# Performance work log

Hardware: AMD Instinct MI355X
Metric: run time of the kernel (lower is better)

The kernel has to match this reference:

```python
import jax, jax.numpy as jnp
import numpy as np
from math import sqrt

B, H, S, D = 4, 16, 2048, 64
NEG = -1000000000.0

def setup_inputs() -> dict:
    key = jax.random.key(0)
    kq, kk, kv, km = jax.random.split(key, 4)
    Q = jax.random.normal(kq, (B, H, S, D), dtype=jnp.float32)
    K = jax.random.normal(kk, (B, H, S, D), dtype=jnp.float32)
    V = jax.random.normal(kv, (B, H, S, D), dtype=jnp.float32)
    mask = jax.random.uniform(km, (B, 1, S, S)) < 0.1
    return {"Q": Q, "K": K, "V": V, "mask": mask}

def reference(Q, K, V, mask) -> jnp.ndarray:
    # scores: [B,H,S,S]
    scores = jnp.einsum('bhqd,bhkd->bhqk', Q, K)
    scores = jnp.where(mask, NEG, scores)
    attn = jax.nn.softmax(scores / sqrt(Q.shape[-1]), axis=-1)
    return jnp.einsum('bhqk,bhkd->bhqd', attn, V)
```

## Files before the change

kernel.cpp:

```cpp
#include <hip/hip_runtime.h>


#define SEQ 2048
#define DIM 64
#define NBH 64
#define LOG2E 1.44269504088896340736f
#define SCL (0.125f * LOG2E)
#define NEG_SCALED -1.25e8f

typedef short bf16x8 __attribute__((ext_vector_type(8)));
typedef float f32x4 __attribute__((ext_vector_type(4)));
typedef float f32x16 __attribute__((ext_vector_type(16)));

static __device__ __forceinline__ unsigned short f2bf(float f) {
    unsigned int u = __float_as_uint(f);
    u += 0x7fffu + ((u >> 16) & 1u);
    return (unsigned short)(u >> 16);
}

#define GLD16(gp, lp) __builtin_amdgcn_global_load_lds( \
    (const __attribute__((address_space(1))) unsigned int*)(gp), \
    (__attribute__((address_space(3))) unsigned int*)(lp), 16, 0, 0)

__global__ __launch_bounds__(256)
void prep_all_kernel(const float* __restrict__ K, const float* __restrict__ V,
                     const int* __restrict__ M,
                     unsigned short* __restrict__ Kb, unsigned short* __restrict__ Vt,
                     unsigned int* __restrict__ Mpt) {
    const int x = blockIdx.x;
    const int t = threadIdx.x;
    if (x < 4096) {
        size_t i0 = ((size_t)x * 256 + t) * 8;
        float4 a = *(const float4*)(K + i0);
        float4 b = *(const float4*)(K + i0 + 4);
        union { uint4 u; unsigned short s[8]; } w;
        w.s[0] = f2bf(a.x); w.s[1] = f2bf(a.y); w.s[2] = f2bf(a.z); w.s[3] = f2bf(a.w);
        w.s[4] = f2bf(b.x); w.s[5] = f2bf(b.y); w.s[6] = f2bf(b.z); w.s[7] = f2bf(b.w);
        *(uint4*)(Kb + i0) = w.u;
    } else if (x < 6144) {
        __shared__ __align__(16) unsigned short T[64 * 64];
        const int vb = x - 4096;
        const int bh = vb >> 5;
        const int k0 = (vb & 31) * 64;
        {
            const int kk = t >> 2;
            const int c  = t & 3;
            const int u  = (kk & ~12) | ((kk & 4) << 1) | ((kk & 8) >> 1);
            const int cs = c ^ ((u >> 3) & 3);
            const float* vp = V + ((size_t)bh * SEQ + k0 + kk) * DIM + c * 16;
            union { uint4 q[2]; unsigned short s[16]; } w;
            #pragma unroll
            for (int j = 0; j < 16; ++j) w.s[j] = f2bf(vp[j]);
            *(uint4*)&T[u * 64 + cs * 16]     = w.q[0];
            *(uint4*)&T[u * 64 + cs * 16 + 8] = w.q[1];
        }
        __syncthreads();
        {
            const int kc = t & 7;
            const int dp = t >> 3;
            const int ch = (dp >> 3) ^ (kc & 3);
            const unsigned int* T32 = (const unsigned int*)T;
            union { uint4 u; unsigned short s[8]; } o0, o1;
            #pragma unroll
            for (int i = 0; i < 8; ++i) {
                unsigned int v = T32[(8 * kc + i) * 32 + ch * 8 + (dp & 7)];
                o0.s[i] = (unsigned short)v;
                o1.s[i] = (unsigned short)(v >> 16);
            }
            unsigned short* op = Vt + ((size_t)bh * DIM + 2 * dp) * SEQ + k0 + 8 * kc;
            *(uint4*)op         = o0.u;
            *(uint4*)(op + SEQ) = o1.u;
        }
    } else {
        __shared__ unsigned int Wt[64][8];
        const int m  = x - 6144;
        const int b  = m >> 8;
        const int q0 = ((m >> 3) & 31) * 64;
        const int k0 = (m & 7) * 256;
        const int w  = t >> 6, l = t & 63;
        #pragma unroll 4
        for (int row = 0; row < 16; ++row) {
            const int q = q0 + w * 16 + row;
            int4 v4 = *(const int4*)(M + ((size_t)b * SEQ + q) * SEQ + k0 + l * 4);
            unsigned int nib = (unsigned int)(v4.x != 0) | ((unsigned int)(v4.y != 0) << 1)
                             | ((unsigned int)(v4.z != 0) << 2) | ((unsigned int)(v4.w != 0) << 3);
            unsigned int v = nib << (4 * (l & 7));
            v |= __shfl_xor(v, 1);
            v |= __shfl_xor(v, 2);
            v |= __shfl_xor(v, 4);
            if ((l & 7) == 0) Wt[w * 16 + row][l >> 3] = v;
        }
        __syncthreads();
        {
            const int q = t & 63, g0 = t >> 6;
            #pragma unroll
            for (int gg = 0; gg < 2; ++gg) {
                const int g = g0 + gg * 4;
                Mpt[((size_t)b * 64 + (k0 >> 5) + g) * SEQ + q0 + q] = Wt[q][g];
            }
        }
    }
}

__global__ __launch_bounds__(256, 4)
void attn_main_kernel(const float* __restrict__ Q,
                      const unsigned short* __restrict__ Kb,
                      const unsigned short* __restrict__ Vt,
                      const unsigned int* __restrict__ Mpt,
                      float* __restrict__ O)
{
    const int bh   = blockIdx.y;
    const int b    = bh >> 4;
    const int q0   = blockIdx.x * 128;
    const int tid  = threadIdx.x;
    const int wave = tid >> 6;
    const int lane = tid & 63;
    const int h    = lane >> 5;
    const int q32  = lane & 31;

    __shared__ __align__(16) unsigned short Kt[2][32 * 64];
    __shared__ __align__(16) unsigned short Vs[2][64 * 32];

    const unsigned short* Kbh = Kb + (size_t)bh * SEQ * DIM;
    const unsigned short* Vbh = Vt + (size_t)bh * SEQ * DIM;

    bf16x8 qf[4];
    {
        const float* qp = Q + ((size_t)bh * SEQ + q0 + wave * 32 + q32) * DIM + h * 8;
        #pragma unroll
        for (int dc = 0; dc < 4; ++dc) {
            float4 xx = *(const float4*)(qp + dc * 16);
            float4 yy = *(const float4*)(qp + dc * 16 + 4);
            qf[dc][0] = (short)f2bf(xx.x * SCL); qf[dc][1] = (short)f2bf(xx.y * SCL);
            qf[dc][2] = (short)f2bf(xx.z * SCL); qf[dc][3] = (short)f2bf(xx.w * SCL);
            qf[dc][4] = (short)f2bf(yy.x * SCL); qf[dc][5] = (short)f2bf(yy.y * SCL);
            qf[dc][6] = (short)f2bf(yy.z * SCL); qf[dc][7] = (short)f2bf(yy.w * SCL);
        }
    }

    const int kkey  = wave * 8 + (lane >> 3);
    const int kclog = (lane & 7) ^ (lane >> 3);
    const unsigned short* kg = Kbh + (size_t)kkey * DIM + kclog * 8;
    const int vd    = wave * 16 + (lane >> 2);
    const int vclog = (lane & 3) ^ ((lane >> 3) & 3);
    const unsigned short* vg = Vbh + (size_t)vd * SEQ + vclog * 8;
    unsigned short* kl[2] = { &Kt[0][wave * 512], &Kt[1][wave * 512] };
    unsigned short* vl[2] = { &Vs[0][wave * 512], &Vs[1][wave * 512] };

    const unsigned int* mp = Mpt + (size_t)b * 64 * SEQ + (q0 + wave * 32 + q32);

    f32x16 acc[2];
    #pragma unroll
    for (int i = 0; i < 16; ++i) { acc[0][i] = 0.f; acc[1][i] = 0.f; }
    float lsum = 0.f;

    GLD16(kg, kl[0]);
    GLD16(vg, vl[0]);

    #pragma unroll 2
    for (int it = 0; it < SEQ / 32; ++it) {
        __syncthreads();

        unsigned int mw = mp[it * SEQ];

        if (it + 1 < SEQ / 32) {
            const unsigned short* kgn = kg + (size_t)(it + 1) * 32 * DIM;
            const unsigned short* vgn = vg + (size_t)(it + 1) * 32;
            int nb = (it + 1) & 1;
            GLD16(kgn, kl[nb]);
            GLD16(vgn, vl[nb]);
        }

        const unsigned short* Ktb = Kt[it & 1];
        const unsigned short* Vsb = Vs[it & 1];

        f32x16 sc;
        #pragma unroll
        for (int i = 0; i < 16; ++i) sc[i] = 0.f;
        #pragma unroll
        for (int dc = 0; dc < 4; ++dc) {
            const int pos = (dc * 2 + h) ^ (q32 & 7);
            bf16x8 kf = *(const bf16x8*)(Ktb + q32 * 64 + pos * 8);
            sc = __builtin_amdgcn_mfma_f32_32x32x16_bf16(kf, qf[dc], sc, 0, 0, 0);
        }

        const unsigned int mq = mw >> (4 * h);
        float pv[16];
        #pragma unroll
        for (int r = 0; r < 16; ++r) {
            const int s = (r & 3) + 8 * (r >> 2);
            float e = __builtin_amdgcn_exp2f(sc[r]);
            pv[r] = ((mq >> s) & 1u) ? 0.f : e;
            lsum += pv[r];
        }
        unsigned int pk[8];
        #pragma unroll
        for (int m = 0; m < 8; ++m) {
            unsigned int u0 = __float_as_uint(pv[2 * m])     + 0x8000u;
            unsigned int u1 = __float_as_uint(pv[2 * m + 1]) + 0x8000u;
            pk[m] = __builtin_amdgcn_perm(u1, u0, 0x07060302u);
        }

        #pragma unroll
        for (int kk = 0; kk < 2; ++kk) {
            union { unsigned int u[4]; bf16x8 v; } fr;
            fr.u[0] = pk[4 * kk + 0];
            fr.u[1] = pk[4 * kk + 1];
            fr.u[2] = pk[4 * kk + 2];
            fr.u[3] = pk[4 * kk + 3];
            #pragma unroll
            for (int dh = 0; dh < 2; ++dh) {
                const int d   = dh * 32 + q32;
                const int pos = (kk * 2 + h) ^ ((q32 >> 1) & 3);
                bf16x8 vf = *(const bf16x8*)(Vsb + d * 32 + pos * 8);
                acc[dh] = __builtin_amdgcn_mfma_f32_32x32x16_bf16(vf, fr.v, acc[dh], 0, 0, 0);
            }
        }
    }

    lsum += __shfl_xor(lsum, 32);
    const float inv = 1.f / lsum;
    float* orow = O + ((size_t)bh * SEQ + q0 + wave * 32 + q32) * DIM;
    #pragma unroll
    for (int dh = 0; dh < 2; ++dh) {
        #pragma unroll
        for (int r23 = 0; r23 < 4; ++r23) {
            float4 w;
            w.x = acc[dh][4 * r23 + 0] * inv;
            w.y = acc[dh][4 * r23 + 1] * inv;
            w.z = acc[dh][4 * r23 + 2] * inv;
            w.w = acc[dh][4 * r23 + 3] * inv;
            *(float4*)(orow + dh * 32 + r23 * 8 + h * 4) = w;
        }
    }
}

__global__ __launch_bounds__(256)
void attn_fallback_kernel(const float* __restrict__ Q,
                          const float* __restrict__ K,
                          const float* __restrict__ V,
                          const int* __restrict__ mask,
                          float* __restrict__ O)
{
    const int bh   = blockIdx.y;
    const int b    = bh >> 4;
    const int q0   = blockIdx.x * 64;
    const int tid  = threadIdx.x;
    const int wave = tid >> 6;
    const int lane = tid & 63;
    const int quad = lane >> 4;
    const int l16  = lane & 15;

    __shared__ __align__(16) unsigned short Klds[32][72];
    __shared__ __align__(16) unsigned short VT[64][40];
    __shared__ __align__(16) unsigned short Plds[4][16][40];

    const float* Qb = Q + (size_t)bh * SEQ * DIM;
    const float* Kb = K + (size_t)bh * SEQ * DIM;
    const float* Vb = V + (size_t)bh * SEQ * DIM;
    const int*   Mb = mask + (size_t)b * SEQ * SEQ;

    const int qrow_frag = q0 + wave * 16 + l16;
    bf16x8 qf0, qf1;
    {
        const float* qp = Qb + (size_t)qrow_frag * DIM + quad * 8;
        #pragma unroll
        for (int i = 0; i < 8; ++i) {
            qf0[i] = (short)f2bf(qp[i]);
            qf1[i] = (short)f2bf(qp[32 + i]);
        }
    }

    f32x4 acc[4];
    #pragma unroll
    for (int dg = 0; dg < 4; ++dg) acc[dg] = (f32x4){0.f, 0.f, 0.f, 0.f};
    float mrowv[4] = {-INFINITY, -INFINITY, -INFINITY, -INFINITY};
    float lrow[4] = {0.f, 0.f, 0.f, 0.f};

    const int skey = tid >> 3;
    const int sd0  = (tid & 7) * 8;
    const int vkey = tid & 31;
    const int vd0  = (tid >> 5) * 8;
    const int qrow_m = q0 + wave * 16 + quad * 4;

    for (int kb = 0; kb < SEQ; kb += 32) {
        __syncthreads();
        {
            const float* kp = Kb + (size_t)(kb + skey) * DIM + sd0;
            union { uint4 u4; unsigned short s[8]; } kw;
            #pragma unroll
            for (int i = 0; i < 8; ++i) kw.s[i] = f2bf(kp[i]);
            *(uint4*)&Klds[skey][sd0] = kw.u4;
        }
        {
            const float* vp = Vb + (size_t)(kb + vkey) * DIM + vd0;
            #pragma unroll
            for (int i = 0; i < 8; ++i) VT[vd0 + i][vkey] = f2bf(vp[i]);
        }
        __syncthreads();

        f32x4 scr[2];
        scr[0] = (f32x4){0.f, 0.f, 0.f, 0.f};
        scr[1] = (f32x4){0.f, 0.f, 0.f, 0.f};
        #pragma unroll
        for (int nt = 0; nt < 2; ++nt) {
            bf16x8 kf0 = *(const bf16x8*)&Klds[nt * 16 + l16][quad * 8];
            bf16x8 kf1 = *(const bf16x8*)&Klds[nt * 16 + l16][32 + quad * 8];
            scr[nt] = __builtin_amdgcn_mfma_f32_16x16x32_bf16(qf0, kf0, scr[nt], 0, 0, 0);
            scr[nt] = __builtin_amdgcn_mfma_f32_16x16x32_bf16(qf1, kf1, scr[nt], 0, 0, 0);
        }

        float x[2][4];
        #pragma unroll
        for (int nt = 0; nt < 2; ++nt)
            #pragma unroll
            for (int r = 0; r < 4; ++r) {
                int mv = Mb[(size_t)(qrow_m + r) * SEQ + kb + nt * 16 + l16];
                x[nt][r] = mv ? NEG_SCALED : scr[nt][r] * 0.125f;
            }

        float p[2][4];
        #pragma unroll
        for (int r = 0; r < 4; ++r) {
            float rm = fmaxf(x[0][r], x[1][r]);
            #pragma unroll
            for (int off = 1; off < 16; off <<= 1)
                rm = fmaxf(rm, __shfl_xor(rm, off, 16));
            float mn = fmaxf(mrowv[r], rm);
            float alpha = exp2f((mrowv[r] - mn) * LOG2E);
            mrowv[r] = mn;
            float p0 = exp2f((x[0][r] - mn) * LOG2E);
            float p1 = exp2f((x[1][r] - mn) * LOG2E);
            p[0][r] = p0; p[1][r] = p1;
            float rs = p0 + p1;
            #pragma unroll
            for (int off = 1; off < 16; off <<= 1)
                rs += __shfl_xor(rs, off, 16);
            lrow[r] = lrow[r] * alpha + rs;
            #pragma unroll
            for (int dg = 0; dg < 4; ++dg)
                acc[dg][r] *= alpha;
        }

        #pragma unroll
        for (int nt = 0; nt < 2; ++nt)
            #pragma unroll
            for (int r = 0; r < 4; ++r)
                Plds[wave][quad * 4 + r][nt * 16 + l16] = f2bf(p[nt][r]);

        bf16x8 pf = *(const bf16x8*)&Plds[wave][l16][quad * 8];

        #pragma unroll
        for (int dg = 0; dg < 4; ++dg) {
            bf16x8 vf = *(const bf16x8*)&VT[dg * 16 + l16][quad * 8];
            acc[dg] = __builtin_amdgcn_mfma_f32_16x16x32_bf16(pf, vf, acc[dg], 0, 0, 0);
        }
    }

    float* Ob = O + (size_t)bh * SEQ * DIM;
    #pragma unroll
    for (int r = 0; r < 4; ++r) {
        float inv = 1.f / lrow[r];
        #pragma unroll
        for (int dg = 0; dg < 4; ++dg)
            Ob[(size_t)(qrow_m + r) * DIM + dg * 16 + l16] = acc[dg][r] * inv;
    }
}

extern "C" void kernel_launch(void* const* d_in, const int* in_sizes, int n_in,
                              void* d_out, int out_size, void* d_ws, size_t ws_size,
                              hipStream_t stream) {
    const float* Q = (const float*)d_in[0];
    const float* K = (const float*)d_in[1];
    const float* V = (const float*)d_in[2];
    const int* mask = (const int*)d_in[3];
    float*        O = (float*)d_out;

    const size_t szK = (size_t)NBH * SEQ * DIM * 2;
    const size_t szV = (size_t)NBH * SEQ * DIM * 2;
    const size_t szM = (size_t)4 * SEQ * (SEQ / 32) * 4;
    const size_t need = szK + szV + szM;

    if (ws_size >= need) {
        unsigned short* Kb = (unsigned short*)d_ws;
        unsigned short* Vt = (unsigned short*)((char*)d_ws + szK);
        unsigned int*  Mpt = (unsigned int*)((char*)d_ws + szK + szV);

        prep_all_kernel<<<dim3(7168), 256, 0, stream>>>(K, V, mask, Kb, Vt, Mpt);
        attn_main_kernel<<<dim3(SEQ / 128, NBH), 256, 0, stream>>>(Q, Kb, Vt, Mpt, O);
    } else {
        attn_fallback_kernel<<<dim3(SEQ / 64, NBH), 256, 0, stream>>>(Q, K, V, mask, O);
    }
}
```

Before: 279.6 us.

## Fold mask into MFMA init, prefetch mask, remap blocks, use packed bf16 convert

The score accumulator now starts at a large negative constant for masked positions, built with a bitfield extract, so the post-exp select disappears. The mask word is prefetched one iteration ahead. Blocks are remapped so neighbouring blocks cover different heads. The row-sum is split across four accumulators, and the bf16 pack uses the hardware v_cvt_pk_bf16_f32 instruction. s_setprio hints are placed around the MFMA sections, and the V transpose prep now reads coalesced float4 loads. Together these cut VALU work and mask-load latency in the main loop, at the cost of the inline asm rounding mode and the block remap possibly changing cache locality.

```diff
diff --git a/kernel.cpp b/kernel.cpp
--- a/kernel.cpp
+++ b/kernel.cpp
@@ -43,16 +43,20 @@
         const int bh = vb >> 5;
         const int k0 = (vb & 31) * 64;
         {
-            const int kk = t >> 2;
-            const int c  = t & 3;
-            const int u  = (kk & ~12) | ((kk & 4) << 1) | ((kk & 8) >> 1);
-            const int cs = c ^ ((u >> 3) & 3);
-            const float* vp = V + ((size_t)bh * SEQ + k0 + kk) * DIM + c * 16;
-            union { uint4 q[2]; unsigned short s[16]; } w;
-            #pragma unroll
-            for (int j = 0; j < 16; ++j) w.s[j] = f2bf(vp[j]);
-            *(uint4*)&T[u * 64 + cs * 16]     = w.q[0];
-            *(uint4*)&T[u * 64 + cs * 16 + 8] = w.q[1];
+            const float* Vb = V + ((size_t)bh * SEQ + k0) * DIM;
+            #pragma unroll
+            for (int j = 0; j < 4; ++j) {
+                const int fi = (j * 256 + t) * 4;
+                const int kk = fi >> 6;
+                const int d0 = fi & 63;
+                float4 f = *(const float4*)(Vb + fi);
+                const int u  = (kk & ~12) | ((kk & 4) << 1) | ((kk & 8) >> 1);
+                const int cs = (d0 >> 4) ^ ((u >> 3) & 3);
+                union { uint2 q; unsigned short s[4]; } w4;
+                w4.s[0] = f2bf(f.x); w4.s[1] = f2bf(f.y);
+                w4.s[2] = f2bf(f.z); w4.s[3] = f2bf(f.w);
+                *(uint2*)&T[u * 64 + cs * 16 + (d0 & 15)] = w4.q;
+            }
         }
         __syncthreads();
         {
@@ -109,14 +113,16 @@
                       const unsigned int* __restrict__ Mpt,
                       float* __restrict__ O)
 {
-    const int bh   = blockIdx.y;
+    const int n    = blockIdx.y * gridDim.x + blockIdx.x;
+    const int bh   = ((n & 7) << 3) | (n >> 7);
+    const int q0   = ((n >> 3) & 15) * 128;
     const int b    = bh >> 4;
-    const int q0   = blockIdx.x * 128;
     const int tid  = threadIdx.x;
     const int wave = tid >> 6;
     const int lane = tid & 63;
     const int h    = lane >> 5;
     const int q32  = lane & 31;
+    const int sh4  = 4 * h;
 
     __shared__ __align__(16) unsigned short Kt[2][32 * 64];
     __shared__ __align__(16) unsigned short Vs[2][64 * 32];
@@ -152,55 +158,66 @@
     f32x16 acc[2];
     #pragma unroll
     for (int i = 0; i < 16; ++i) { acc[0][i] = 0.f; acc[1][i] = 0.f; }
-    float lsum = 0.f;
+    float ls0 = 0.f, ls1 = 0.f, ls2 = 0.f, ls3 = 0.f;
 
     GLD16(kg, kl[0]);
     GLD16(vg, vl[0]);
+    unsigned int mw = mp[0];
 
     #pragma unroll 2
     for (int it = 0; it < SEQ / 32; ++it) {
         __syncthreads();
 
-        unsigned int mw = mp[it * SEQ];
-
+        unsigned int mw_n = 0;
         if (it + 1 < SEQ / 32) {
             const unsigned short* kgn = kg + (size_t)(it + 1) * 32 * DIM;
             const unsigned short* vgn = vg + (size_t)(it + 1) * 32;
             int nb = (it + 1) & 1;
             GLD16(kgn, kl[nb]);
             GLD16(vgn, vl[nb]);
+            mw_n = mp[(it + 1) * SEQ];
         }
 
         const unsigned short* Ktb = Kt[it & 1];
         const unsigned short* Vsb = Vs[it & 1];
 
+        const unsigned int mq = mw >> sh4;
         f32x16 sc;
         #pragma unroll
-        for (int i = 0; i < 16; ++i) sc[i] = 0.f;
+        for (int r = 0; r < 16; ++r) {
+            const int s = (r & 3) + 8 * (r >> 2);
+            sc[r] = __int_as_float(__builtin_amdgcn_sbfe(mq, s, 1) & 0xC2C80000u);
+        }
+
+        __builtin_amdgcn_s_setprio(1);
         #pragma unroll
         for (int dc = 0; dc < 4; ++dc) {
             const int pos = (dc * 2 + h) ^ (q32 & 7);
             bf16x8 kf = *(const bf16x8*)(Ktb + q32 * 64 + pos * 8);
             sc = __builtin_amdgcn_mfma_f32_32x32x16_bf16(kf, qf[dc], sc, 0, 0, 0);
         }
-
-        const unsigned int mq = mw >> (4 * h);
+        __builtin_amdgcn_s_setprio(0);
+
         float pv[16];
         #pragma unroll
-        for (int r = 0; r < 16; ++r) {
-            const int s = (r & 3) + 8 * (r >> 2);
-            float e = __builtin_amdgcn_exp2f(sc[r]);
-            pv[r] = ((mq >> s) & 1u) ? 0.f : e;
-            lsum += pv[r];
-        }
+        for (int r = 0; r < 16; ++r) pv[r] = __builtin_amdgcn_exp2f(sc[r]);
+
+        #pragma unroll
+        for (int r = 0; r < 16; r += 4) {
+            ls0 += pv[r + 0];
+            ls1 += pv[r + 1];
+            ls2 += pv[r + 2];
+            ls3 += pv[r + 3];
+        }
+
         unsigned int pk[8];
         #pragma unroll
         for (int m = 0; m < 8; ++m) {
-            unsigned int u0 = __float_as_uint(pv[2 * m])     + 0x8000u;
-            unsigned int u1 = __float_as_uint(pv[2 * m + 1]) + 0x8000u;
-            pk[m] = __builtin_amdgcn_perm(u1, u0, 0x07060302u);
-        }
-
+            asm("v_cvt_pk_bf16_f32 %0, %1, %2"
+                : "=v"(pk[m]) : "v"(pv[2 * m]), "v"(pv[2 * m + 1]));
+        }
+
+        __builtin_amdgcn_s_setprio(1);
         #pragma unroll
         for (int kk = 0; kk < 2; ++kk) {
             union { unsigned int u[4]; bf16x8 v; } fr;
@@ -216,8 +233,12 @@
                 acc[dh] = __builtin_amdgcn_mfma_f32_32x32x16_bf16(vf, fr.v, acc[dh], 0, 0, 0);
             }
         }
-    }
-
+        __builtin_amdgcn_s_setprio(0);
+
+        mw = mw_n;
+    }
+
+    float lsum = (ls0 + ls1) + (ls2 + ls3);
     lsum += __shfl_xor(lsum, 32);
     const float inv = 1.f / lsum;
     float* orow = O + ((size_t)bh * SEQ + q0 + wave * 32 + q32) * DIM;
```

Result: faster. 270.6 us (-3.2%).
